# Optimization experiments

Measured on AMD Instinct MI355X. Metric: run time of the kernel, lower is better.

The kernel has to match this reference:

```python
import jax, jax.numpy as jnp
import numpy as np

D_MODEL = 1024
NUM_HEADS = 16
D_K = D_MODEL // NUM_HEADS


def setup_inputs() -> dict:
    key = jax.random.key(0)
    ks = jax.random.split(key, 5)
    s = 1.0 / np.sqrt(D_MODEL)
    return {
        "x": jax.random.normal(ks[0], (2, 2048, D_MODEL), dtype=jnp.float32),
        "Wq": jax.random.normal(ks[1], (D_MODEL, D_MODEL), dtype=jnp.float32) * s,
        "bq": jnp.zeros((D_MODEL,), jnp.float32),
        "Wk": jax.random.normal(ks[2], (D_MODEL, D_MODEL), dtype=jnp.float32) * s,
        "bk": jnp.zeros((D_MODEL,), jnp.float32),
        "Wv": jax.random.normal(ks[3], (D_MODEL, D_MODEL), dtype=jnp.float32) * s,
        "bv": jnp.zeros((D_MODEL,), jnp.float32),
        "Wo": jax.random.normal(ks[4], (D_MODEL, D_MODEL), dtype=jnp.float32) * s,
        "bo": jnp.zeros((D_MODEL,), jnp.float32),
    }


def reference(x, Wq, bq, Wk, bk, Wv, bv, Wo, bo):
    B, S, _ = x.shape

    def split_heads(t):  # [B,S,D] -> [B,H,S,d_k]
        return t.reshape(B, S, NUM_HEADS, D_K).transpose(0, 2, 1, 3)

    q = split_heads(x @ Wq + bq)
    k = split_heads(x @ Wk + bk)
    v = split_heads(x @ Wv + bv)

    # [B,H,S,S] scores, scaled by 1/sqrt(d_k)
    scores = jnp.einsum("bhqd,bhkd->bhqk", q, k) / jnp.sqrt(jnp.float32(D_K))
    causal = jnp.tril(jnp.ones((S, S), dtype=bool))  # True = keep
    scores = jnp.where(causal, scores, -jnp.inf)
    attn = jax.nn.softmax(scores, axis=-1)
    # dropout is identity in eval mode
    out = jnp.einsum("bhqk,bhkd->bhqd", attn, v)
    out = out.transpose(0, 2, 1, 3).reshape(B, S, D_MODEL)
    return out @ Wo + bo
```

## Files before the change

kernel.cpp:

```cpp
#include <hip/hip_runtime.h>
#include <stdint.h>

typedef __attribute__((ext_vector_type(8))) short bf16x8;
typedef __attribute__((ext_vector_type(8))) unsigned short ushort8;
typedef __attribute__((ext_vector_type(4))) float f32x4;
typedef __attribute__((ext_vector_type(16))) float f32x16;

constexpr int DM = 1024;
constexpr int SQ = 2048;
constexpr int NB = 2;
constexpr int NH = 16;
constexpr int DK = 64;
constexpr int M  = NB * SQ;

__device__ inline float bf2f(unsigned short u) {
    union { uint32_t i; float f; } c; c.i = ((uint32_t)u) << 16; return c.f;
}
__device__ inline unsigned short f2bf(float f) {
    union { float f; uint32_t i; } c; c.f = f;
    uint32_t r = c.i + 0x7FFFu + ((c.i >> 16) & 1u);
    return (unsigned short)(r >> 16);
}
__device__ inline float exp2v(float x) {
    float r;
    asm("v_exp_f32 %0, %1" : "=v"(r) : "v"(x));
    return r;
}
__device__ inline uint32_t cvtpk(float lo, float hi) {
    uint32_t r;
    asm("v_cvt_pk_bf16_f32 %0, %1, %2" : "=v"(r) : "v"(lo), "v"(hi));
    return r;
}
__device__ inline uint32_t sx32(uint32_t v) {
    return (uint32_t)__shfl_xor((int)v, 32);
}
__device__ inline bf16x8 mkfrag(uint32_t a, uint32_t b, uint32_t c, uint32_t d) {
    union { bf16x8 v; uint32_t u[4]; } m;
    m.u[0] = a; m.u[1] = b; m.u[2] = c; m.u[3] = d;
    return m.v;
}
__device__ inline void gload_lds16(const unsigned short* g, unsigned short* l) {
    __builtin_amdgcn_global_load_lds(
        (const __attribute__((address_space(1))) void*)g,
        (__attribute__((address_space(3))) void*)l, 16, 0, 0);
}

__global__ __launch_bounds__(256) void cvt_x(const float* __restrict__ x,
                                             unsigned short* __restrict__ xb) {
    int idx = (blockIdx.x * 256 + threadIdx.x) * 8;
    const float* p = x + idx;
    ushort8 o;
#pragma unroll
    for (int i = 0; i < 8; ++i) o[i] = f2bf(p[i]);
    *(ushort8*)(xb + idx) = o;
}

__global__ __launch_bounds__(256) void cvt_w(const float* __restrict__ W,
                                             unsigned short* __restrict__ Wt) {
    __shared__ float tile[32][33];
    int tx = threadIdx.x, ty = threadIdx.y;
    int bx = blockIdx.x, by = blockIdx.y;
#pragma unroll
    for (int j = 0; j < 4; ++j)
        tile[ty + j * 8][tx] = W[(size_t)(by * 32 + ty + j * 8) * DM + bx * 32 + tx];
    __syncthreads();
#pragma unroll
    for (int j = 0; j < 4; ++j)
        Wt[(size_t)(bx * 32 + ty + j * 8) * DM + by * 32 + tx] = f2bf(tile[tx][ty + j * 8]);
}

template <int MODE>
__global__ __launch_bounds__(256) void gemm128(const unsigned short* __restrict__ A,
                                               const unsigned short* __restrict__ Bt,
                                               const float* __restrict__ b0,
                                               const float* __restrict__ b1,
                                               const float* __restrict__ b2,
                                               void* __restrict__ outp) {
    constexpr int K = 1024;
    __shared__ __align__(16) unsigned short As[128 * 32];
    __shared__ __align__(16) unsigned short Bs[128 * 32];
    const int t = threadIdx.x;
    const int w = t >> 6, l = t & 63;
    const int l15 = l & 15, lg = l >> 4;
    const int wr = w >> 1, wc = w & 1;
    const int bx = blockIdx.x, by = blockIdx.y;

    f32x4 acc[4][4] = {};

    const int srow = l >> 2;
    const int sk   = (l & 3) * 8;
    const unsigned short* Abase = A  + (size_t)(by * 128) * K;
    const unsigned short* Bbase = Bt + (size_t)(bx * 128) * K;

    for (int k0 = 0; k0 < K; k0 += 32) {
#pragma unroll
        for (int i = 0; i < 2; ++i) {
            const int row = w * 32 + i * 16 + srow;
            gload_lds16(Abase + (size_t)row * K + k0 + sk, &As[row * 32 + sk]);
            gload_lds16(Bbase + (size_t)row * K + k0 + sk, &Bs[row * 32 + sk]);
        }
        __syncthreads();

        bf16x8 af[4], bfr[4];
#pragma unroll
        for (int mi = 0; mi < 4; ++mi)
            af[mi] = *(const bf16x8*)&As[(wr * 64 + mi * 16 + l15) * 32 + lg * 8];
#pragma unroll
        for (int ni = 0; ni < 4; ++ni)
            bfr[ni] = *(const bf16x8*)&Bs[(wc * 64 + ni * 16 + l15) * 32 + lg * 8];
#pragma unroll
        for (int mi = 0; mi < 4; ++mi)
#pragma unroll
            for (int ni = 0; ni < 4; ++ni)
                acc[mi][ni] = __builtin_amdgcn_mfma_f32_16x16x32_bf16(af[mi], bfr[ni], acc[mi][ni], 0, 0, 0);
        __syncthreads();
    }

#pragma unroll
    for (int ni = 0; ni < 4; ++ni) {
        const int n = bx * 128 + wc * 64 + ni * 16 + l15;
        float bias;
        if constexpr (MODE == 0) {
            const int mat = n >> 10;
            const float* bp = (mat == 0) ? b0 : (mat == 1) ? b1 : b2;
            bias = bp[n & 1023];
        } else {
            bias = b0[n];
        }
#pragma unroll
        for (int mi = 0; mi < 4; ++mi)
#pragma unroll
            for (int i = 0; i < 4; ++i) {
                const int m = by * 128 + wr * 64 + mi * 16 + lg * 4 + i;
                float v = acc[mi][ni][i] + bias;
                if constexpr (MODE == 0) {
                    const int mat = n >> 10, c = n & 1023;
                    if (mat == 0) v *= 0.18033688f;
                    const int h = c >> 6, d = c & 63;
                    const int b = m >> 11, si = m & 2047;
                    size_t idx;
                    if (mat == 2)
                        idx = ((size_t)(b * NH + h) * DK + d) * SQ + si;
                    else
                        idx = ((size_t)(b * NH + h) * SQ + si) * DK + d;
                    ((unsigned short*)outp)[(size_t)mat * (NB * NH * SQ * DK) + idx] = f2bf(v);
                } else {
                    ((float*)outp)[(size_t)m * DM + n] = v;
                }
            }
    }
}

__global__ __launch_bounds__(64) void attn32(const unsigned short* __restrict__ Qg,
                                             const unsigned short* __restrict__ Kg,
                                             const unsigned short* __restrict__ Vtg,
                                             unsigned short* __restrict__ O) {
    __shared__ __align__(16) char Ks0[8192];
    __shared__ __align__(16) char Vs0[8192];
    const float NEG_INF = -__builtin_inff();

    const int bid = blockIdx.x;
    const int bh  = bid & 31;
    const int g   = bid >> 5;
    const int base_i = (g & 7) * 4 + (g >> 4);
    const int qi  = (g & 8) ? (63 - base_i) : base_i;
    const int Tlast = qi >> 1;
    const int b = bh >> 4, h = bh & 15;
    const size_t base = (size_t)bh * SQ * DK;

    const int l = threadIdx.x;
    const int l31 = l & 31, hi = l >> 5;
    const bool h0 = (hi == 0);

    const int lrow = l >> 3;
    const int lchunk = (l & 7) ^ lrow;
    const unsigned short* ksrc0 = Kg + base + (size_t)lrow * DK + lchunk * 8;
    const unsigned short* vsrc0 = Vtg + (size_t)(bh * 64 + lrow) * SQ + lchunk * 8;

    int roff[4];
#pragma unroll
    for (int c = 0; c < 4; ++c) roff[c] = (hi * 16 + 32 * c) ^ ((l & 7) << 4);
    const int rb0 = l31 * 128, rb1 = (32 + l31) * 128;

    const int qrow = qi * 32 + l31;

    bf16x8 qf[4];
    {
        const unsigned short* qp = Qg + base + (size_t)qrow * DK + hi * 8;
#pragma unroll
        for (int c = 0; c < 4; ++c) qf[c] = *(const bf16x8*)(qp + 16 * c);
    }

    float mrun = NEG_INF, lsum = 0.f;
    f32x16 o0 = {}, o1 = {};

#pragma unroll 1
    for (int kt = 0; kt <= Tlast; ++kt) {
        {
            const unsigned short* ks = ksrc0 + (size_t)kt * 64 * DK;
            const unsigned short* vs = vsrc0 + kt * 64;
#pragma unroll
            for (int i = 0; i < 8; ++i)
                gload_lds16(ks + i * 8 * DK, (unsigned short*)Ks0 + i * 512 + l * 8);
#pragma unroll
            for (int i = 0; i < 8; ++i)
                gload_lds16(vs + (size_t)i * 8 * SQ, (unsigned short*)Vs0 + i * 512 + l * 8);
        }
        __syncthreads();

        f32x16 s0v = {}, s1v = {};
#pragma unroll
        for (int c = 0; c < 4; ++c) {
            bf16x8 ka0 = *(const bf16x8*)(Ks0 + rb0 + roff[c]);
            bf16x8 ka1 = *(const bf16x8*)(Ks0 + rb1 + roff[c]);
            s0v = __builtin_amdgcn_mfma_f32_32x32x16_bf16(ka0, qf[c], s0v, 0, 0, 0);
            s1v = __builtin_amdgcn_mfma_f32_32x32x16_bf16(ka1, qf[c], s1v, 0, 0, 0);
        }

        float s[32];
#pragma unroll
        for (int r = 0; r < 16; ++r) { s[r] = s0v[r]; s[16 + r] = s1v[r]; }
        if (kt == Tlast) {
            const int qrel = qrow - kt * 64;
#pragma unroll
            for (int r = 0; r < 16; ++r) {
                const int key0 = (r & 3) + 8 * (r >> 2) + 4 * hi;
                if (key0 > qrel) s[r] = NEG_INF;
                if (key0 + 32 > qrel) s[16 + r] = NEG_INF;
            }
        }

        float t8[8];
#pragma unroll
        for (int i = 0; i < 8; ++i)
            t8[i] = fmaxf(fmaxf(s[i], s[i + 8]), fmaxf(s[i + 16], s[i + 24]));
        float tm = fmaxf(fmaxf(fmaxf(t8[0], t8[1]), fmaxf(t8[2], t8[3])),
                         fmaxf(fmaxf(t8[4], t8[5]), fmaxf(t8[6], t8[7])));
        tm = fmaxf(tm, __shfl_xor(tm, 32));

        const float mn = fmaxf(mrun, tm);
        if (!__all(tm - mrun <= 11.0f)) {
            const float corr = exp2v(mrun - mn);
            lsum *= corr;
#pragma unroll
            for (int r = 0; r < 16; ++r) { o0[r] *= corr; o1[r] *= corr; }
            mrun = mn;
        }

#pragma unroll
        for (int r = 0; r < 32; ++r) s[r] = exp2v(s[r] - mrun);
        float a8[8];
#pragma unroll
        for (int i = 0; i < 8; ++i)
            a8[i] = (s[i] + s[i + 8]) + (s[i + 16] + s[i + 24]);
        lsum += ((a8[0] + a8[1]) + (a8[2] + a8[3])) + ((a8[4] + a8[5]) + (a8[6] + a8[7]));

        uint32_t pk[16];
#pragma unroll
        for (int i = 0; i < 16; ++i) pk[i] = cvtpk(s[2 * i], s[2 * i + 1]);
        const uint32_t X1 = sx32(h0 ? pk[2]  : pk[0]);
        const uint32_t X2 = sx32(h0 ? pk[3]  : pk[1]);
        const uint32_t X3 = sx32(h0 ? pk[6]  : pk[4]);
        const uint32_t X4 = sx32(h0 ? pk[7]  : pk[5]);
        const uint32_t X5 = sx32(h0 ? pk[10] : pk[8]);
        const uint32_t X6 = sx32(h0 ? pk[11] : pk[9]);
        const uint32_t X7 = sx32(h0 ? pk[14] : pk[12]);
        const uint32_t X8 = sx32(h0 ? pk[15] : pk[13]);
        bf16x8 pf[4];
        pf[0] = mkfrag(h0 ? pk[0]  : X1, h0 ? pk[1]  : X2, h0 ? X1 : pk[2],  h0 ? X2 : pk[3]);
        pf[1] = mkfrag(h0 ? pk[4]  : X3, h0 ? pk[5]  : X4, h0 ? X3 : pk[6],  h0 ? X4 : pk[7]);
        pf[2] = mkfrag(h0 ? pk[8]  : X5, h0 ? pk[9]  : X6, h0 ? X5 : pk[10], h0 ? X6 : pk[11]);
        pf[3] = mkfrag(h0 ? pk[12] : X7, h0 ? pk[13] : X8, h0 ? X7 : pk[14], h0 ? X8 : pk[15]);

#pragma unroll
        for (int vi = 0; vi < 4; ++vi) {
            bf16x8 va0 = *(const bf16x8*)(Vs0 + rb0 + roff[vi]);
            bf16x8 va1 = *(const bf16x8*)(Vs0 + rb1 + roff[vi]);
            o0 = __builtin_amdgcn_mfma_f32_32x32x16_bf16(va0, pf[vi], o0, 0, 0, 0);
            o1 = __builtin_amdgcn_mfma_f32_32x32x16_bf16(va1, pf[vi], o1, 0, 0, 0);
        }
    }

    lsum += __shfl_xor(lsum, 32);
    const float inv = 1.f / lsum;
    unsigned short* op = O + ((size_t)(b * SQ + qrow)) * DM + h * 64;
#pragma unroll
    for (int r = 0; r < 16; r += 2) {
        const int d = (r & 3) + 8 * (r >> 2) + 4 * hi;
        uint32_t w0 = (uint32_t)f2bf(o0[r] * inv) | ((uint32_t)f2bf(o0[r + 1] * inv) << 16);
        uint32_t w1 = (uint32_t)f2bf(o1[r] * inv) | ((uint32_t)f2bf(o1[r + 1] * inv) << 16);
        *(uint32_t*)(op + d) = w0;
        *(uint32_t*)(op + 32 + d) = w1;
    }
}

extern "C" void kernel_launch(void* const* d_in, const int* in_sizes, int n_in,
                              void* d_out, int out_size, void* d_ws, size_t ws_size,
                              hipStream_t stream) {
    const float* x  = (const float*)d_in[0];
    const float* Wq = (const float*)d_in[1];
    const float* bq = (const float*)d_in[2];
    const float* Wk = (const float*)d_in[3];
    const float* bk = (const float*)d_in[4];
    const float* Wv = (const float*)d_in[5];
    const float* bv = (const float*)d_in[6];
    const float* Wo = (const float*)d_in[7];
    const float* bo = (const float*)d_in[8];
    float* out = (float*)d_out;

    char* ws = (char*)d_ws;
    const size_t XB_BYTES = (size_t)M * DM * 2;
    const size_t W_BYTES  = (size_t)DM * DM * 2;
    const size_t H_BYTES  = (size_t)NB * NH * SQ * DK * 2;
    unsigned short* xb  = (unsigned short*)ws;
    unsigned short* wqt = (unsigned short*)(ws + XB_BYTES);
    unsigned short* wkt = (unsigned short*)(ws + XB_BYTES + W_BYTES);
    unsigned short* wvt = (unsigned short*)(ws + XB_BYTES + 2 * W_BYTES);
    unsigned short* wot = (unsigned short*)(ws + XB_BYTES + 3 * W_BYTES);
    unsigned short* Qb  = (unsigned short*)(ws + XB_BYTES + 4 * W_BYTES);
    unsigned short* Kb  = (unsigned short*)(ws + XB_BYTES + 4 * W_BYTES + H_BYTES);
    unsigned short* Vb  = (unsigned short*)(ws + XB_BYTES + 4 * W_BYTES + 2 * H_BYTES);

    cvt_x<<<(M * DM) / (256 * 8), 256, 0, stream>>>(x, xb);
    dim3 wgrid(32, 32), wblk(32, 8);
    cvt_w<<<wgrid, wblk, 0, stream>>>(Wq, wqt);
    cvt_w<<<wgrid, wblk, 0, stream>>>(Wk, wkt);
    cvt_w<<<wgrid, wblk, 0, stream>>>(Wv, wvt);
    cvt_w<<<wgrid, wblk, 0, stream>>>(Wo, wot);

    gemm128<0><<<dim3(24, 32), 256, 0, stream>>>(xb, wqt, bq, bk, bv, Qb);

    attn32<<<NB * NH * 64, 64, 0, stream>>>(Qb, Kb, Vb, xb );

    gemm128<1><<<dim3(8, 32), 256, 0, stream>>>(xb, wot, bo, bo, bo, out);
}
```

Before: 142.6 us.

## Split attention KV loop across two waves and pair causal query tiles per block

The attention kernel now runs two wavefronts per block. They split the key tiles (even and odd) for the same 32-row query tile and merge their partial softmax state (max, sum, output) through LDS at the end. Each block also handles a complementary pair of query tiles (pr and 63-pr), which balances causal work and halves the grid. This aims to shorten the per-query serial KV loop and balance load, at the cost of extra barriers, an LDS reduction, and a lost load-overlap opportunity when one wave idles on an odd tile count.

```diff
diff --git a/kernel.cpp b/kernel.cpp
--- a/kernel.cpp
+++ b/kernel.cpp
@@ -151,26 +151,28 @@
     }
 }
 
-__global__ __launch_bounds__(64) void attn32(const unsigned short* __restrict__ Qg,
-                                             const unsigned short* __restrict__ Kg,
-                                             const unsigned short* __restrict__ Vtg,
-                                             unsigned short* __restrict__ O) {
-    __shared__ __align__(16) char Ks0[8192];
-    __shared__ __align__(16) char Vs0[8192];
+__global__ __launch_bounds__(128) void attn32(const unsigned short* __restrict__ Qg,
+                                              const unsigned short* __restrict__ Kg,
+                                              const unsigned short* __restrict__ Vtg,
+                                              unsigned short* __restrict__ O) {
+    __shared__ __align__(16) char KV[2][16384];
     const float NEG_INF = -__builtin_inff();
 
     const int bid = blockIdx.x;
     const int bh  = bid & 31;
-    const int g   = bid >> 5;
-    const int base_i = (g & 7) * 4 + (g >> 4);
-    const int qi  = (g & 8) ? (63 - base_i) : base_i;
-    const int Tlast = qi >> 1;
+    const int pr  = bid >> 5;
     const int b = bh >> 4, h = bh & 15;
     const size_t base = (size_t)bh * SQ * DK;
 
-    const int l = threadIdx.x;
+    const int t = threadIdx.x;
+    const int w = t >> 6, l = t & 63;
     const int l31 = l & 31, hi = l >> 5;
     const bool h0 = (hi == 0);
+
+    char* Ks0 = KV[w];
+    char* Vs0 = KV[w] + 8192;
+    float* myP = (float*)KV[w];
+    float* otP = (float*)KV[w ^ 1];
 
     const int lrow = l >> 3;
     const int lchunk = (l & 7) ^ lrow;
@@ -182,115 +184,149 @@
     for (int c = 0; c < 4; ++c) roff[c] = (hi * 16 + 32 * c) ^ ((l & 7) << 4);
     const int rb0 = l31 * 128, rb1 = (32 + l31) * 128;
 
-    const int qrow = qi * 32 + l31;
-
-    bf16x8 qf[4];
-    {
-        const unsigned short* qp = Qg + base + (size_t)qrow * DK + hi * 8;
-#pragma unroll
-        for (int c = 0; c < 4; ++c) qf[c] = *(const bf16x8*)(qp + 16 * c);
-    }
-
-    float mrun = NEG_INF, lsum = 0.f;
-    f32x16 o0 = {}, o1 = {};
-
 #pragma unroll 1
-    for (int kt = 0; kt <= Tlast; ++kt) {
+    for (int half = 0; half < 2; ++half) {
+        const int qi   = half ? (63 - pr) : pr;
+        const int T    = (qi >> 1) + 1;
+        const int Tmax = (T + 1) >> 1;
+        const int qrow = qi * 32 + l31;
+
+        bf16x8 qf[4];
         {
-            const unsigned short* ks = ksrc0 + (size_t)kt * 64 * DK;
-            const unsigned short* vs = vsrc0 + kt * 64;
-#pragma unroll
-            for (int i = 0; i < 8; ++i)
-                gload_lds16(ks + i * 8 * DK, (unsigned short*)Ks0 + i * 512 + l * 8);
-#pragma unroll
-            for (int i = 0; i < 8; ++i)
-                gload_lds16(vs + (size_t)i * 8 * SQ, (unsigned short*)Vs0 + i * 512 + l * 8);
+            const unsigned short* qp = Qg + base + (size_t)qrow * DK + hi * 8;
+#pragma unroll
+            for (int c = 0; c < 4; ++c) qf[c] = *(const bf16x8*)(qp + 16 * c);
+        }
+
+        float mrun = NEG_INF, lsum = 0.f;
+        f32x16 o0 = {}, o1 = {};
+
+#pragma unroll 1
+        for (int i = 0; i < Tmax; ++i) {
+            const int kt = 2 * i + w;
+            const bool act = kt < T;
+            if (act) {
+                const unsigned short* ks = ksrc0 + (size_t)kt * 64 * DK;
+                const unsigned short* vs = vsrc0 + kt * 64;
+#pragma unroll
+                for (int j = 0; j < 8; ++j)
+                    gload_lds16(ks + j * 8 * DK, (unsigned short*)Ks0 + j * 512 + l * 8);
+#pragma unroll
+                for (int j = 0; j < 8; ++j)
+                    gload_lds16(vs + (size_t)j * 8 * SQ, (unsigned short*)Vs0 + j * 512 + l * 8);
+            }
+            __syncthreads();
+            if (!act) continue;
+
+            f32x16 s0v = {}, s1v = {};
+#pragma unroll
+            for (int c = 0; c < 4; ++c) {
+                bf16x8 ka0 = *(const bf16x8*)(Ks0 + rb0 + roff[c]);
+                bf16x8 ka1 = *(const bf16x8*)(Ks0 + rb1 + roff[c]);
+                s0v = __builtin_amdgcn_mfma_f32_32x32x16_bf16(ka0, qf[c], s0v, 0, 0, 0);
+                s1v = __builtin_amdgcn_mfma_f32_32x32x16_bf16(ka1, qf[c], s1v, 0, 0, 0);
+            }
+
+            float s[32];
+#pragma unroll
+            for (int r = 0; r < 16; ++r) { s[r] = s0v[r]; s[16 + r] = s1v[r]; }
+            if (kt == T - 1) {
+                const int qrel = qrow - kt * 64;
+#pragma unroll
+                for (int r = 0; r < 16; ++r) {
+                    const int key0 = (r & 3) + 8 * (r >> 2) + 4 * hi;
+                    if (key0 > qrel) s[r] = NEG_INF;
+                    if (key0 + 32 > qrel) s[16 + r] = NEG_INF;
+                }
+            }
+
+            float t8[8];
+#pragma unroll
+            for (int j = 0; j < 8; ++j)
+                t8[j] = fmaxf(fmaxf(s[j], s[j + 8]), fmaxf(s[j + 16], s[j + 24]));
+            float tm = fmaxf(fmaxf(fmaxf(t8[0], t8[1]), fmaxf(t8[2], t8[3])),
+                             fmaxf(fmaxf(t8[4], t8[5]), fmaxf(t8[6], t8[7])));
+            tm = fmaxf(tm, __shfl_xor(tm, 32));
+
+            const float mn = fmaxf(mrun, tm);
+            if (!__all(tm - mrun <= 11.0f)) {
+                const float corr = exp2v(mrun - mn);
+                lsum *= corr;
+#pragma unroll
+                for (int r = 0; r < 16; ++r) { o0[r] *= corr; o1[r] *= corr; }
+                mrun = mn;
+            }
+
+#pragma unroll
+            for (int r = 0; r < 32; ++r) s[r] = exp2v(s[r] - mrun);
+            float a8[8];
+#pragma unroll
+            for (int j = 0; j < 8; ++j)
+                a8[j] = (s[j] + s[j + 8]) + (s[j + 16] + s[j + 24]);
+            lsum += ((a8[0] + a8[1]) + (a8[2] + a8[3])) + ((a8[4] + a8[5]) + (a8[6] + a8[7]));
+
+            uint32_t pk[16];
+#pragma unroll
+            for (int j = 0; j < 16; ++j) pk[j] = cvtpk(s[2 * j], s[2 * j + 1]);
+            const uint32_t X1 = sx32(h0 ? pk[2]  : pk[0]);
+            const uint32_t X2 = sx32(h0 ? pk[3]  : pk[1]);
+            const uint32_t X3 = sx32(h0 ? pk[6]  : pk[4]);
+            const uint32_t X4 = sx32(h0 ? pk[7]  : pk[5]);
+            const uint32_t X5 = sx32(h0 ? pk[10] : pk[8]);
+            const uint32_t X6 = sx32(h0 ? pk[11] : pk[9]);
+            const uint32_t X7 = sx32(h0 ? pk[14] : pk[12]);
+            const uint32_t X8 = sx32(h0 ? pk[15] : pk[13]);
+            bf16x8 pf[4];
+            pf[0] = mkfrag(h0 ? pk[0]  : X1, h0 ? pk[1]  : X2, h0 ? X1 : pk[2],  h0 ? X2 : pk[3]);
+            pf[1] = mkfrag(h0 ? pk[4]  : X3, h0 ? pk[5]  : X4, h0 ? X3 : pk[6],  h0 ? X4 : pk[7]);
+            pf[2] = mkfrag(h0 ? pk[8]  : X5, h0 ? pk[9]  : X6, h0 ? X5 : pk[10], h0 ? X6 : pk[11]);
+            pf[3] = mkfrag(h0 ? pk[12] : X7, h0 ? pk[13] : X8, h0 ? X7 : pk[14], h0 ? X8 : pk[15]);
+
+#pragma unroll
+            for (int vi = 0; vi < 4; ++vi) {
+                bf16x8 va0 = *(const bf16x8*)(Vs0 + rb0 + roff[vi]);
+                bf16x8 va1 = *(const bf16x8*)(Vs0 + rb1 + roff[vi]);
+                o0 = __builtin_amdgcn_mfma_f32_32x32x16_bf16(va0, pf[vi], o0, 0, 0, 0);
+                o1 = __builtin_amdgcn_mfma_f32_32x32x16_bf16(va1, pf[vi], o1, 0, 0, 0);
+            }
+        }
+
+        lsum += __shfl_xor(lsum, 32);
+        {
+            float* pb = myP + (size_t)l * 40;
+#pragma unroll
+            for (int r = 0; r < 16; ++r) { pb[r] = o0[r]; pb[16 + r] = o1[r]; }
+            pb[32] = mrun; pb[33] = lsum;
         }
         __syncthreads();
-
-        f32x16 s0v = {}, s1v = {};
-#pragma unroll
-        for (int c = 0; c < 4; ++c) {
-            bf16x8 ka0 = *(const bf16x8*)(Ks0 + rb0 + roff[c]);
-            bf16x8 ka1 = *(const bf16x8*)(Ks0 + rb1 + roff[c]);
-            s0v = __builtin_amdgcn_mfma_f32_32x32x16_bf16(ka0, qf[c], s0v, 0, 0, 0);
-            s1v = __builtin_amdgcn_mfma_f32_32x32x16_bf16(ka1, qf[c], s1v, 0, 0, 0);
-        }
-
-        float s[32];
-#pragma unroll
-        for (int r = 0; r < 16; ++r) { s[r] = s0v[r]; s[16 + r] = s1v[r]; }
-        if (kt == Tlast) {
-            const int qrel = qrow - kt * 64;
+        float lm;
+        {
+            const float* qb = otP + (size_t)l * 40;
+            const float pm = qb[32], pl = qb[33];
+            const float mm = fmaxf(mrun, pm);
+            const float ca = exp2v(mrun - mm);
+            const float cb = exp2v(pm - mm);
+            lm = lsum * ca + pl * cb;
 #pragma unroll
             for (int r = 0; r < 16; ++r) {
-                const int key0 = (r & 3) + 8 * (r >> 2) + 4 * hi;
-                if (key0 > qrel) s[r] = NEG_INF;
-                if (key0 + 32 > qrel) s[16 + r] = NEG_INF;
-            }
-        }
-
-        float t8[8];
-#pragma unroll
-        for (int i = 0; i < 8; ++i)
-            t8[i] = fmaxf(fmaxf(s[i], s[i + 8]), fmaxf(s[i + 16], s[i + 24]));
-        float tm = fmaxf(fmaxf(fmaxf(t8[0], t8[1]), fmaxf(t8[2], t8[3])),
-                         fmaxf(fmaxf(t8[4], t8[5]), fmaxf(t8[6], t8[7])));
-        tm = fmaxf(tm, __shfl_xor(tm, 32));
-
-        const float mn = fmaxf(mrun, tm);
-        if (!__all(tm - mrun <= 11.0f)) {
-            const float corr = exp2v(mrun - mn);
-            lsum *= corr;
-#pragma unroll
-            for (int r = 0; r < 16; ++r) { o0[r] *= corr; o1[r] *= corr; }
-            mrun = mn;
-        }
-
-#pragma unroll
-        for (int r = 0; r < 32; ++r) s[r] = exp2v(s[r] - mrun);
-        float a8[8];
-#pragma unroll
-        for (int i = 0; i < 8; ++i)
-            a8[i] = (s[i] + s[i + 8]) + (s[i + 16] + s[i + 24]);
-        lsum += ((a8[0] + a8[1]) + (a8[2] + a8[3])) + ((a8[4] + a8[5]) + (a8[6] + a8[7]));
-
-        uint32_t pk[16];
-#pragma unroll
-        for (int i = 0; i < 16; ++i) pk[i] = cvtpk(s[2 * i], s[2 * i + 1]);
-        const uint32_t X1 = sx32(h0 ? pk[2]  : pk[0]);
-        const uint32_t X2 = sx32(h0 ? pk[3]  : pk[1]);
-        const uint32_t X3 = sx32(h0 ? pk[6]  : pk[4]);
-        const uint32_t X4 = sx32(h0 ? pk[7]  : pk[5]);
-        const uint32_t X5 = sx32(h0 ? pk[10] : pk[8]);
-        const uint32_t X6 = sx32(h0 ? pk[11] : pk[9]);
-        const uint32_t X7 = sx32(h0 ? pk[14] : pk[12]);
-        const uint32_t X8 = sx32(h0 ? pk[15] : pk[13]);
-        bf16x8 pf[4];
-        pf[0] = mkfrag(h0 ? pk[0]  : X1, h0 ? pk[1]  : X2, h0 ? X1 : pk[2],  h0 ? X2 : pk[3]);
-        pf[1] = mkfrag(h0 ? pk[4]  : X3, h0 ? pk[5]  : X4, h0 ? X3 : pk[6],  h0 ? X4 : pk[7]);
-        pf[2] = mkfrag(h0 ? pk[8]  : X5, h0 ? pk[9]  : X6, h0 ? X5 : pk[10], h0 ? X6 : pk[11]);
-        pf[3] = mkfrag(h0 ? pk[12] : X7, h0 ? pk[13] : X8, h0 ? X7 : pk[14], h0 ? X8 : pk[15]);
-
-#pragma unroll
-        for (int vi = 0; vi < 4; ++vi) {
-            bf16x8 va0 = *(const bf16x8*)(Vs0 + rb0 + roff[vi]);
-            bf16x8 va1 = *(const bf16x8*)(Vs0 + rb1 + roff[vi]);
-            o0 = __builtin_amdgcn_mfma_f32_32x32x16_bf16(va0, pf[vi], o0, 0, 0, 0);
-            o1 = __builtin_amdgcn_mfma_f32_32x32x16_bf16(va1, pf[vi], o1, 0, 0, 0);
-        }
-    }
-
-    lsum += __shfl_xor(lsum, 32);
-    const float inv = 1.f / lsum;
-    unsigned short* op = O + ((size_t)(b * SQ + qrow)) * DM + h * 64;
-#pragma unroll
-    for (int r = 0; r < 16; r += 2) {
-        const int d = (r & 3) + 8 * (r >> 2) + 4 * hi;
-        uint32_t w0 = (uint32_t)f2bf(o0[r] * inv) | ((uint32_t)f2bf(o0[r + 1] * inv) << 16);
-        uint32_t w1 = (uint32_t)f2bf(o1[r] * inv) | ((uint32_t)f2bf(o1[r + 1] * inv) << 16);
-        *(uint32_t*)(op + d) = w0;
-        *(uint32_t*)(op + 32 + d) = w1;
+                o0[r] = o0[r] * ca + qb[r] * cb;
+                o1[r] = o1[r] * ca + qb[16 + r] * cb;
+            }
+        }
+        __syncthreads();
+
+        if (w == half) {
+            const float inv = 1.f / lm;
+            unsigned short* op = O + ((size_t)(b * SQ + qrow)) * DM + h * 64;
+#pragma unroll
+            for (int r = 0; r < 16; r += 2) {
+                const int d = (r & 3) + 8 * (r >> 2) + 4 * hi;
+                uint32_t w0 = (uint32_t)f2bf(o0[r] * inv) | ((uint32_t)f2bf(o0[r + 1] * inv) << 16);
+                uint32_t w1 = (uint32_t)f2bf(o1[r] * inv) | ((uint32_t)f2bf(o1[r + 1] * inv) << 16);
+                *(uint32_t*)(op + d) = w0;
+                *(uint32_t*)(op + 32 + d) = w1;
+            }
+        }
     }
 }
 
@@ -330,7 +366,7 @@
 
     gemm128<0><<<dim3(24, 32), 256, 0, stream>>>(xb, wqt, bq, bk, bv, Qb);
 
-    attn32<<<NB * NH * 64, 64, 0, stream>>>(Qb, Kb, Vb, xb );
+    attn32<<<NB * NH * 32, 128, 0, stream>>>(Qb, Kb, Vb, xb );
 
     gemm128<1><<<dim3(8, 32), 256, 0, stream>>>(xb, wot, bo, bo, bo, out);
 }
```

Result: faster. 129.2 us (-9.4%).
